# Optimization experiments

Measured on AMD Instinct MI355X. Metric: run time of the kernel, lower is better.

## Reference

```python
import jax, jax.numpy as jnp
import numpy as np

NPOINT = 1024
RADIUS = 0.2
NSAMPLE = 32
EPS = 1e-5


def farthest_point_sample(xyz, npoint):
    # xyz: [B, N, 3] -> [B, npoint] int32, deterministic start at index 0
    B, N, _ = xyz.shape

    def step(carry, _):
        dist, farthest = carry
        centroid = jnp.take_along_axis(xyz, farthest[:, None, None], axis=1)  # [B,1,3]
        d = jnp.sum((xyz - centroid) ** 2, axis=-1)  # [B,N]
        dist = jnp.minimum(dist, d)
        nxt = jnp.argmax(dist, axis=-1).astype(jnp.int32)
        return (dist, nxt), farthest

    init = (jnp.full((B, N), 1e10, dtype=xyz.dtype), jnp.zeros((B,), dtype=jnp.int32))
    _, idxs = jax.lax.scan(step, init, None, length=npoint)
    return idxs.T  # [B, npoint]


def query_ball_point(radius, nsample, xyz, new_xyz):
    # xyz: [B,N,3], new_xyz: [B,S,3] -> [B,S,nsample] int32
    N = xyz.shape[1]
    sqr = jnp.sum((new_xyz[:, :, None, :] - xyz[:, None, :, :]) ** 2, axis=-1)  # [B,S,N]
    ar = jnp.arange(N, dtype=jnp.int32)
    gidx = jnp.where(sqr > radius ** 2, N, ar[None, None, :])
    gidx = jnp.sort(gidx, axis=-1)[:, :, :nsample]  # sorts index values, matching torch
    first = gidx[:, :, :1]
    return jnp.where(gidx == N, first, gidx)


def mlp_layer(h, w, b, g, be, m, v):
    # h: [B, Cin, K, S]; 1x1 Conv2d + BatchNorm2d(eval) + ReLU
    h = jnp.einsum('oc,bcks->boks', w, h) + b[None, :, None, None]
    h = (h - m[None, :, None, None]) * (g[None, :, None, None] / jnp.sqrt(v[None, :, None, None] + EPS)) + be[None, :, None, None]
    return jax.nn.relu(h)


def setup_inputs() -> dict:
    key = jax.random.key(0)
    ks = jax.random.split(key, 24)
    inp = {
        'xyz': jax.random.normal(ks[0], (1, 16, 3, 4096), jnp.float32),
        'points': jax.random.normal(ks[1], (1, 16, 64, 4096), jnp.float32),
        'w0': jax.random.normal(ks[2], (64, 67), jnp.float32) * 0.1,
        'b0': jax.random.normal(ks[3], (64,), jnp.float32) * 0.1,
        'g0': jax.random.uniform(ks[4], (64,), jnp.float32),
        'be0': jax.random.normal(ks[5], (64,), jnp.float32) * 0.1,
        'm0': jax.random.normal(ks[6], (64,), jnp.float32) * 0.1,
        'v0': jax.random.uniform(ks[7], (64,), jnp.float32),
        'w1': jax.random.normal(ks[8], (64, 64), jnp.float32) * 0.1,
        'b1': jax.random.normal(ks[9], (64,), jnp.float32) * 0.1,
        'g1': jax.random.uniform(ks[10], (64,), jnp.float32),
        'be1': jax.random.normal(ks[11], (64,), jnp.float32) * 0.1,
        'm1': jax.random.normal(ks[12], (64,), jnp.float32) * 0.1,
        'v1': jax.random.uniform(ks[13], (64,), jnp.float32),
        'w2': jax.random.normal(ks[14], (128, 64), jnp.float32) * 0.1,
        'b2': jax.random.normal(ks[15], (128,), jnp.float32) * 0.1,
        'g2': jax.random.uniform(ks[16], (128,), jnp.float32),
        'be2': jax.random.normal(ks[17], (128,), jnp.float32) * 0.1,
        'm2': jax.random.normal(ks[18], (128,), jnp.float32) * 0.1,
        'v2': jax.random.uniform(ks[19], (128,), jnp.float32),
    }
    return inp


def reference(xyz, points, w0, b0, g0, be0, m0, v0, w1, b1, g1, be1, m1, v1, w2, b2, g2, be2, m2, v2):
    T, B, C, N = xyz.shape
    BT = T * B
    x = xyz.reshape(BT, C, N).transpose(0, 2, 1)          # [B', N, 3]
    p = points.reshape(BT, -1, N).transpose(0, 2, 1)      # [B', N, D]

    fps_idx = farthest_point_sample(x, NPOINT)            # [B', S]
    bidx = jnp.arange(BT)[:, None]
    new_xyz = x[bidx, fps_idx]                            # [B', S, 3]

    idx = query_ball_point(RADIUS, NSAMPLE, x, new_xyz)   # [B', S, K]
    b3 = jnp.arange(BT)[:, None, None]
    grouped_xyz = x[b3, idx]                              # [B', S, K, 3]
    grouped_norm = grouped_xyz - new_xyz[:, :, None, :]
    grouped_p = p[b3, idx]                                # [B', S, K, D]
    new_points = jnp.concatenate([grouped_norm, grouped_p], axis=-1)  # [B', S, K, 3+D]

    h = new_points.transpose(0, 3, 2, 1)                  # [B', 3+D, K, S]
    h = mlp_layer(h, w0, b0, g0, be0, m0, v0)
    h = mlp_layer(h, w1, b1, g1, be1, m1, v1)
    h = mlp_layer(h, w2, b2, g2, be2, m2, v2)
    out = jnp.max(h, axis=2)                              # [B', Cout, S]

    new_xyz_out = new_xyz.transpose(0, 2, 1).reshape(T, B, C, NPOINT)
    return new_xyz_out, out
```

## Files before the change

### kernel.cpp

```cpp
#include <hip/hip_runtime.h>
#include <hip/hip_bf16.h>

#define NPTS    4096
#define NBATCH  16
#define NPOINT  1024
#define NSAMPLE 32

typedef float v2f __attribute__((ext_vector_type(2)));

#define ROW_SHR1  0x111
#define ROW_SHR2  0x112
#define ROW_SHR4  0x114
#define ROW_SHR8  0x118
#define ROW_BC15  0x142
#define ROW_BC31  0x143

template<int CTRL>
__device__ __forceinline__ unsigned dpp_mov(unsigned v) {
    return (unsigned)__builtin_amdgcn_update_dpp(0, (int)v, CTRL, 0xF, 0xF, true);
}
template<int CTRL>
__device__ __forceinline__ float dpp_maxf(float v) {
    unsigned t = dpp_mov<CTRL>(__float_as_uint(v));
    return fmaxf(v, __uint_as_float(t));
}

__device__ void u_role(int g, const float* __restrict__ points,
                       const float* __restrict__ w0, float* __restrict__ U)
{
    const int b = g >> 12, p = g & (NPTS - 1);
    const float* pb = points + (size_t)b * 64 * NPTS + p;
    float in[64];
    #pragma unroll
    for (int c = 0; c < 64; ++c) in[c] = pb[c * NPTS];

    float* ug = U + (size_t)g * 64;
    for (int o4 = 0; o4 < 64; o4 += 4) {
        const float* r0 = w0 + (o4+0)*67 + 3;
        const float* r1 = w0 + (o4+1)*67 + 3;
        const float* r2 = w0 + (o4+2)*67 + 3;
        const float* r3 = w0 + (o4+3)*67 + 3;
        float a0 = 0.f, a1 = 0.f, a2 = 0.f, a3 = 0.f;
        #pragma unroll
        for (int c = 0; c < 64; ++c) {
            const float x = in[c];
            a0 = fmaf(r0[c], x, a0);
            a1 = fmaf(r1[c], x, a1);
            a2 = fmaf(r2[c], x, a2);
            a3 = fmaf(r3[c], x, a3);
        }
        *(float4*)(ug + o4) = make_float4(a0, a1, a2, a3);
    }
}

__device__ void setup_role(
    const float* __restrict__ w0, const float* __restrict__ b0,
    const float* __restrict__ g0, const float* __restrict__ be0,
    const float* __restrict__ m0, const float* __restrict__ v0,
    const float* __restrict__ w1, const float* __restrict__ b1,
    const float* __restrict__ g1, const float* __restrict__ be1,
    const float* __restrict__ m1, const float* __restrict__ v1,
    const float* __restrict__ b2, const float* __restrict__ g2,
    const float* __restrict__ be2, const float* __restrict__ m2,
    const float* __restrict__ v2, float* __restrict__ wp)
{
    const int t = threadIdx.x;
    for (int i = t; i < 3*64; i += 256) {
        int k = i >> 6, o = i & 63;
        wp[i] = w0[o*67 + k];
    }
    for (int i = t; i < 64*64; i += 256) {
        int o = i >> 6, k = i & 63;
        wp[192 + k*64 + o] = w1[i];
    }
    if (t < 64) {
        float s0 = g0[t] / sqrtf(v0[t] + 1e-5f);
        wp[4288 + t] = s0;
        wp[4352 + t] = (b0[t] - m0[t]) * s0 + be0[t];
        float s1 = g1[t] / sqrtf(v1[t] + 1e-5f);
        wp[4416 + t] = s1;
        wp[4480 + t] = (b1[t] - m1[t]) * s1 + be1[t];
    }
    if (t < 128) {
        float s2 = g2[t] / sqrtf(v2[t] + 1e-5f);
        wp[4544 + t] = s2;
        wp[4672 + t] = (b2[t] - m2[t]) * s2 + be2[t];
    }
}

__global__ __launch_bounds__(256) void fps_fused_kernel(
    const float* __restrict__ xyz, const float* __restrict__ points,
    const float* __restrict__ w0, const float* __restrict__ b0,
    const float* __restrict__ g0, const float* __restrict__ be0,
    const float* __restrict__ m0, const float* __restrict__ v0,
    const float* __restrict__ w1, const float* __restrict__ b1,
    const float* __restrict__ g1, const float* __restrict__ be1,
    const float* __restrict__ m1, const float* __restrict__ v1,
    const float* __restrict__ b2, const float* __restrict__ g2,
    const float* __restrict__ be2, const float* __restrict__ m2,
    const float* __restrict__ v2,
    float* __restrict__ newxyz, float* __restrict__ U, float* __restrict__ wp)
{
    #pragma clang fp contract(off)
    if (blockIdx.x >= 16) {
        if (blockIdx.x < 272) {
            u_role((blockIdx.x - 16) * 256 + threadIdx.x, points, w0, U);
        } else {
            setup_role(w0,b0,g0,be0,m0,v0, w1,b1,g1,be1,m1,v1,
                       b2,g2,be2,m2,v2, wp);
        }
        return;
    }

    const int b    = blockIdx.x;
    const int tid  = threadIdx.x;
    const int lane = tid & 63;
    const int w    = tid >> 6;
    const float* xb = xyz + (size_t)b * 3 * NPTS;

    __shared__ float4 P[NPTS];
    __shared__ unsigned long long slotk[2][4];
    __shared__ float4 slotc[2][4];

    v2f px2[8], py2[8], pz2[8], dist2[8];
    #pragma unroll
    for (int q = 0; q < 4; ++q) {
        const int n4 = tid * 16 + q * 4;
        float4 xs = *(const float4*)(xb + n4);
        float4 ys = *(const float4*)(xb + NPTS + n4);
        float4 zs = *(const float4*)(xb + 2*NPTS + n4);
        px2[2*q+0] = (v2f){xs.x, xs.y}; px2[2*q+1] = (v2f){xs.z, xs.w};
        py2[2*q+0] = (v2f){ys.x, ys.y}; py2[2*q+1] = (v2f){ys.z, ys.w};
        pz2[2*q+0] = (v2f){zs.x, zs.y}; pz2[2*q+1] = (v2f){zs.z, zs.w};
        P[n4+0] = make_float4(xs.x, ys.x, zs.x, 0.f);
        P[n4+1] = make_float4(xs.y, ys.y, zs.y, 0.f);
        P[n4+2] = make_float4(xs.z, ys.z, zs.z, 0.f);
        P[n4+3] = make_float4(xs.w, ys.w, zs.w, 0.f);
    }
    #pragma unroll
    for (int j = 0; j < 8; ++j) dist2[j] = (v2f){1e10f, 1e10f};
    __syncthreads();

    float4 c0 = P[0];
    float cx = c0.x, cy = c0.y, cz = c0.z;
    if (tid == 0) {
        newxyz[b*3*NPOINT + 0]        = cx;
        newxyz[b*3*NPOINT + NPOINT]   = cy;
        newxyz[b*3*NPOINT + 2*NPOINT] = cz;
    }

    for (int i = 1; i < NPOINT; ++i) {
        const int s = i & 1;
        const v2f cx2 = (v2f){cx, cx};
        const v2f cy2 = (v2f){cy, cy};
        const v2f cz2 = (v2f){cz, cz};
        float bv = -1.0f; int bj = 0;
        #pragma unroll
        for (int j2 = 0; j2 < 8; ++j2) {
            v2f dx = px2[j2] - cx2;
            v2f dy = py2[j2] - cy2;
            v2f dz = pz2[j2] - cz2;
            v2f xx = dx*dx, yy = dy*dy, zz = dz*dz;
            v2f dd = (xx + yy) + zz;
            v2f nd;
            nd.x = fminf(dist2[j2].x, dd.x);
            nd.y = fminf(dist2[j2].y, dd.y);
            dist2[j2] = nd;
            if (nd.x > bv) { bv = nd.x; bj = 2*j2; }
            if (nd.y > bv) { bv = nd.y; bj = 2*j2+1; }
        }
        const int myidx = (tid << 4) | bj;

        float wv = bv;
        wv = dpp_maxf<ROW_SHR1>(wv);
        wv = dpp_maxf<ROW_SHR2>(wv);
        wv = dpp_maxf<ROW_SHR4>(wv);
        wv = dpp_maxf<ROW_SHR8>(wv);
        wv = dpp_maxf<ROW_BC15>(wv);
        wv = dpp_maxf<ROW_BC31>(wv);
        float wmax = __uint_as_float(
            (unsigned)__builtin_amdgcn_readlane((int)__float_as_uint(wv), 63));
        unsigned long long mask = __ballot(bv == wmax);
        int L = (int)__builtin_ctzll(mask);
        int widx = __builtin_amdgcn_readlane(myidx, L);

        float4 cand = P[widx];
        if (lane == 0) {
            slotk[s][w] = ((unsigned long long)__float_as_uint(wmax) << 32) |
                          (unsigned long long)(unsigned)(~widx);
            slotc[s][w] = cand;
        }
        __syncthreads();

        unsigned long long k0 = slotk[s][0], k1 = slotk[s][1];
        unsigned long long k2 = slotk[s][2], k3 = slotk[s][3];
        float4 s0 = slotc[s][0], s1 = slotc[s][1];
        float4 s2 = slotc[s][2], s3 = slotc[s][3];
        bool b01 = k1 > k0;
        unsigned long long ka = b01 ? k1 : k0;
        float ax = b01 ? s1.x : s0.x, ay = b01 ? s1.y : s0.y, az = b01 ? s1.z : s0.z;
        bool b23 = k3 > k2;
        unsigned long long kb = b23 ? k3 : k2;
        float bx = b23 ? s3.x : s2.x, by = b23 ? s3.y : s2.y, bz = b23 ? s3.z : s2.z;
        bool ab = kb > ka;
        cx = ab ? bx : ax; cy = ab ? by : ay; cz = ab ? bz : az;

        if (tid == 0) {
            newxyz[b*3*NPOINT + i]            = cx;
            newxyz[b*3*NPOINT + NPOINT + i]   = cy;
            newxyz[b*3*NPOINT + 2*NPOINT + i] = cz;
        }
    }
}

__global__ __launch_bounds__(256) void ball_kernel(
    const float* __restrict__ xyz, const float* __restrict__ newxyz,
    int* __restrict__ ball_idx)
{
    const int gid  = blockIdx.x * 256 + threadIdx.x;
    const int wid  = gid >> 6;
    const int lane = threadIdx.x & 63;
    const int b    = wid >> 10;
    const int m    = wid & (NPOINT - 1);
    const float r2 = (float)(0.2 * 0.2);

    const float* xb = xyz + (size_t)b * 3 * NPTS;
    const float cx = newxyz[b*3*NPOINT + m];
    const float cy = newxyz[b*3*NPOINT + NPOINT + m];
    const float cz = newxyz[b*3*NPOINT + 2*NPOINT + m];
    int* out = ball_idx + (size_t)wid * NSAMPLE;

    int base = 0, first = 0;
    for (int c0 = 0; c0 < NPTS; c0 += 64) {
        const int n = c0 + lane;
        float dx = xb[n] - cx, dy = xb[NPTS+n] - cy, dz = xb[2*NPTS+n] - cz;
        float d = __fadd_rn(__fadd_rn(__fmul_rn(dx,dx), __fmul_rn(dy,dy)),
                            __fmul_rn(dz,dz));
        bool inb = (d <= r2);
        unsigned long long mask = __ballot(inb);
        if (base == 0 && mask != 0ull) first = c0 + (int)__builtin_ctzll(mask);
        int pos = base + __popcll(mask & ((1ull << lane) - 1ull));
        if (inb && pos < NSAMPLE) out[pos] = n;
        base += __popcll(mask);
        if (base >= NSAMPLE) break;
    }
    if (lane < NSAMPLE && lane >= base) out[lane] = first;
}

__global__ __launch_bounds__(256) void mlp_kernel(
    const float* __restrict__ xyz, const float* __restrict__ newxyz,
    const int* __restrict__ ball_idx, const float* __restrict__ U,
    const float* __restrict__ wp, const float* __restrict__ w2,
    float* __restrict__ out)
{
    const int col = blockIdx.x * 256 + threadIdx.x;
    const int m   = (col >> 5) & (NPOINT - 1);
    const int b   = col >> 15;
    const int p   = ball_idx[col];

    const float* xb = xyz + (size_t)b * 3 * NPTS;
    const float n0 = xb[p]          - newxyz[b*3*NPOINT + m];
    const float n1 = xb[NPTS + p]   - newxyz[b*3*NPOINT + NPOINT + m];
    const float n2 = xb[2*NPTS + p] - newxyz[b*3*NPOINT + 2*NPOINT + m];

    const float* w0t3 = wp;
    const float* w1t  = wp + 192;
    const float* sc0  = wp + 4288;
    const float* sh0  = wp + 4352;
    const float* sc1  = wp + 4416;
    const float* sh1  = wp + 4480;
    const float* sc2  = wp + 4544;
    const float* sh2  = wp + 4672;

    float h[64];
    const float4* Up = (const float4*)(U + ((size_t)((b << 12) | p)) * 64);
    #pragma unroll
    for (int q = 0; q < 16; ++q) {
        float4 u = Up[q];
        h[4*q+0] = u.x; h[4*q+1] = u.y; h[4*q+2] = u.z; h[4*q+3] = u.w;
    }
    #pragma unroll
    for (int o = 0; o < 64; ++o) h[o] = fmaf(w0t3[o],       n0, h[o]);
    #pragma unroll
    for (int o = 0; o < 64; ++o) h[o] = fmaf(w0t3[64 + o],  n1, h[o]);
    #pragma unroll
    for (int o = 0; o < 64; ++o) h[o] = fmaf(w0t3[128 + o], n2, h[o]);
    #pragma unroll
    for (int o = 0; o < 64; ++o)
        h[o] = fmaxf(fmaf(h[o], sc0[o], sh0[o]), 0.0f);

    float g[64];
    #pragma unroll
    for (int o = 0; o < 64; ++o) g[o] = 0.0f;
    #pragma unroll
    for (int k = 0; k < 64; ++k) {
        const float x = h[k];
        #pragma unroll
        for (int o = 0; o < 64; ++o) g[o] = fmaf(w1t[k*64 + o], x, g[o]);
    }
    #pragma unroll
    for (int o = 0; o < 64; ++o)
        g[o] = fmaxf(fmaf(g[o], sc1[o], sh1[o]), 0.0f);

    float* outb = out + (size_t)b * 128 * NPOINT + m;
    #pragma unroll 2
    for (int o = 0; o < 128; ++o) {
        float acc = 0.0f;
        const float* wr = w2 + o * 64;
        #pragma unroll
        for (int k = 0; k < 64; ++k) acc = fmaf(wr[k], g[k], acc);
        acc = fmaxf(fmaf(acc, sc2[o], sh2[o]), 0.0f);
        acc = dpp_maxf<ROW_SHR1>(acc);
        acc = dpp_maxf<ROW_SHR2>(acc);
        acc = dpp_maxf<ROW_SHR4>(acc);
        acc = dpp_maxf<ROW_SHR8>(acc);
        acc = dpp_maxf<ROW_BC15>(acc);
        if ((threadIdx.x & 31) == 31) outb[o * NPOINT] = acc;
    }
}

extern "C" void kernel_launch(void* const* d_in, const int* in_sizes, int n_in,
                              void* d_out, int out_size, void* d_ws, size_t ws_size,
                              hipStream_t stream)
{
    const float* xyz    = (const float*)d_in[0];
    const float* points = (const float*)d_in[1];
    const float* w0  = (const float*)d_in[2];
    const float* b0  = (const float*)d_in[3];
    const float* g0  = (const float*)d_in[4];
    const float* be0 = (const float*)d_in[5];
    const float* m0  = (const float*)d_in[6];
    const float* v0  = (const float*)d_in[7];
    const float* w1  = (const float*)d_in[8];
    const float* b1  = (const float*)d_in[9];
    const float* g1  = (const float*)d_in[10];
    const float* be1 = (const float*)d_in[11];
    const float* m1  = (const float*)d_in[12];
    const float* v1  = (const float*)d_in[13];
    const float* w2  = (const float*)d_in[14];
    const float* b2  = (const float*)d_in[15];
    const float* g2  = (const float*)d_in[16];
    const float* be2 = (const float*)d_in[17];
    const float* m2  = (const float*)d_in[18];
    const float* v2  = (const float*)d_in[19];

    float* out0 = (float*)d_out;
    float* out1 = out0 + NBATCH * 3 * NPOINT;

    float* U    = (float*)d_ws;
    int*   ball = (int*)((char*)d_ws + (size_t)NBATCH*NPTS*64*sizeof(float));
    float* wp   = (float*)((char*)ball + (size_t)NBATCH*NPOINT*NSAMPLE*sizeof(int));

    hipLaunchKernelGGL(fps_fused_kernel, dim3(273), dim3(256), 0, stream,
                       xyz, points, w0,b0,g0,be0,m0,v0, w1,b1,g1,be1,m1,v1,
                       b2,g2,be2,m2,v2, out0, U, wp);
    hipLaunchKernelGGL(ball_kernel, dim3(NBATCH*NPOINT/4), dim3(256), 0, stream,
                       xyz, out0, ball);
    hipLaunchKernelGGL(mlp_kernel,  dim3(NBATCH*NPOINT*NSAMPLE/256), dim3(256), 0, stream,
                       xyz, out0, ball, U, wp, w2, out1);
}
```

Baseline: 1.003 ms.

## Fuse FPS, ball query and MLP into one persistent producer-consumer kernel

Merges the three kernels into a single persistent launch. Sixteen blocks run farthest-point sampling at raised priority and publish progress counters. The other 240 blocks compute U and the weight setup, wait at a grid barrier, then take work items from an atomic queue. Each item spin-waits until its centroids are ready, then does the ball query into shared memory and the MLP. This overlaps the serial FPS phase with the ball query and MLP, and removes the ball-index round trip through global memory. In exchange it depends on all 256 blocks being co-resident and on cross-block atomics and spin-waits.

Result: slower. 1.047 ms (+4.3%).

```diff
diff --git a/kernel.cpp b/kernel.cpp
--- a/kernel.cpp
+++ b/kernel.cpp
@@ -7,6 +7,7 @@
 #define NSAMPLE 32
 
 typedef float v2f __attribute__((ext_vector_type(2)));
+typedef unsigned long long ull;
 
 #define ROW_SHR1  0x111
 #define ROW_SHR2  0x112
@@ -24,6 +25,11 @@
     unsigned t = dpp_mov<CTRL>(__float_as_uint(v));
     return fmaxf(v, __uint_as_float(t));
 }
+
+#define CTRL_DONE  16
+#define CTRL_QHEAD 17
+#define NCONS      240
+#define NITEMS     2048
 
 __device__ void u_role(int g, const float* __restrict__ points,
                        const float* __restrict__ w0, float* __restrict__ U)
@@ -88,234 +94,270 @@
     }
 }
 
-__global__ __launch_bounds__(256) void fps_fused_kernel(
+__global__ __launch_bounds__(256) void fused_kernel(
     const float* __restrict__ xyz, const float* __restrict__ points,
     const float* __restrict__ w0, const float* __restrict__ b0,
     const float* __restrict__ g0, const float* __restrict__ be0,
-    const float* __restrict__ m0, const float* __restrict__ v0,
+    const float* __restrict__ m0w, const float* __restrict__ v0,
     const float* __restrict__ w1, const float* __restrict__ b1,
     const float* __restrict__ g1, const float* __restrict__ be1,
-    const float* __restrict__ m1, const float* __restrict__ v1,
-    const float* __restrict__ b2, const float* __restrict__ g2,
-    const float* __restrict__ be2, const float* __restrict__ m2,
-    const float* __restrict__ v2,
-    float* __restrict__ newxyz, float* __restrict__ U, float* __restrict__ wp)
+    const float* __restrict__ m1w, const float* __restrict__ v1,
+    const float* __restrict__ w2, const float* __restrict__ b2,
+    const float* __restrict__ g2, const float* __restrict__ be2,
+    const float* __restrict__ m2w, const float* __restrict__ v2,
+    float* __restrict__ newxyz, float* __restrict__ out1,
+    float* __restrict__ U, float* __restrict__ wp, int* __restrict__ ctrl)
 {
     #pragma clang fp contract(off)
-    if (blockIdx.x >= 16) {
-        if (blockIdx.x < 272) {
-            u_role((blockIdx.x - 16) * 256 + threadIdx.x, points, w0, U);
-        } else {
-            setup_role(w0,b0,g0,be0,m0,v0, w1,b1,g1,be1,m1,v1,
-                       b2,g2,be2,m2,v2, wp);
+    __shared__ __align__(16) char smem[65728];
+    __shared__ int item_s;
+
+    if (blockIdx.x < 16) {
+        __builtin_amdgcn_s_setprio(2);
+        float4* P     = reinterpret_cast<float4*>(smem);
+        ull*    slotk = reinterpret_cast<ull*>(smem + 65536);
+        float4* slotc = reinterpret_cast<float4*>(smem + 65600);
+
+        const int b    = blockIdx.x;
+        const int tid  = threadIdx.x;
+        const int lane = tid & 63;
+        const int w    = tid >> 6;
+        const float* xb = xyz + (size_t)b * 3 * NPTS;
+
+        v2f px2[8], py2[8], pz2[8], dist2[8];
+        #pragma unroll
+        for (int q = 0; q < 4; ++q) {
+            const int n4 = tid * 16 + q * 4;
+            float4 xs = *(const float4*)(xb + n4);
+            float4 ys = *(const float4*)(xb + NPTS + n4);
+            float4 zs = *(const float4*)(xb + 2*NPTS + n4);
+            px2[2*q+0] = (v2f){xs.x, xs.y}; px2[2*q+1] = (v2f){xs.z, xs.w};
+            py2[2*q+0] = (v2f){ys.x, ys.y}; py2[2*q+1] = (v2f){ys.z, ys.w};
+            pz2[2*q+0] = (v2f){zs.x, zs.y}; pz2[2*q+1] = (v2f){zs.z, zs.w};
+            P[n4+0] = make_float4(xs.x, ys.x, zs.x, 0.f);
+            P[n4+1] = make_float4(xs.y, ys.y, zs.y, 0.f);
+            P[n4+2] = make_float4(xs.z, ys.z, zs.z, 0.f);
+            P[n4+3] = make_float4(xs.w, ys.w, zs.w, 0.f);
+        }
+        #pragma unroll
+        for (int j = 0; j < 8; ++j) dist2[j] = (v2f){1e10f, 1e10f};
+        __syncthreads();
+
+        float4 c0 = P[0];
+        float cx = c0.x, cy = c0.y, cz = c0.z;
+        if (tid == 0) {
+            newxyz[b*3*NPOINT + 0]        = cx;
+            newxyz[b*3*NPOINT + NPOINT]   = cy;
+            newxyz[b*3*NPOINT + 2*NPOINT] = cz;
+        }
+
+        for (int i = 1; i < NPOINT; ++i) {
+            const int s = i & 1;
+            const v2f cx2 = (v2f){cx, cx};
+            const v2f cy2 = (v2f){cy, cy};
+            const v2f cz2 = (v2f){cz, cz};
+            float bv = -1.0f; int bj = 0;
+            #pragma unroll
+            for (int j2 = 0; j2 < 8; ++j2) {
+                v2f dx = px2[j2] - cx2;
+                v2f dy = py2[j2] - cy2;
+                v2f dz = pz2[j2] - cz2;
+                v2f xx = dx*dx, yy = dy*dy, zz = dz*dz;
+                v2f dd = (xx + yy) + zz;
+                v2f nd;
+                nd.x = fminf(dist2[j2].x, dd.x);
+                nd.y = fminf(dist2[j2].y, dd.y);
+                dist2[j2] = nd;
+                if (nd.x > bv) { bv = nd.x; bj = 2*j2; }
+                if (nd.y > bv) { bv = nd.y; bj = 2*j2+1; }
+            }
+            const int myidx = (tid << 4) | bj;
+
+            float wv = bv;
+            wv = dpp_maxf<ROW_SHR1>(wv);
+            wv = dpp_maxf<ROW_SHR2>(wv);
+            wv = dpp_maxf<ROW_SHR4>(wv);
+            wv = dpp_maxf<ROW_SHR8>(wv);
+            wv = dpp_maxf<ROW_BC15>(wv);
+            wv = dpp_maxf<ROW_BC31>(wv);
+            float wmax = __uint_as_float(
+                (unsigned)__builtin_amdgcn_readlane((int)__float_as_uint(wv), 63));
+            ull mask = __ballot(bv == wmax);
+            int L = (int)__builtin_ctzll(mask);
+            int widx = __builtin_amdgcn_readlane(myidx, L);
+
+            float4 cand = P[widx];
+            if (lane == 0) {
+                slotk[s*4 + w] = ((ull)__float_as_uint(wmax) << 32) |
+                                 (ull)(unsigned)(~widx);
+                slotc[s*4 + w] = cand;
+            }
+            __syncthreads();
+
+            ull k0 = slotk[s*4+0], k1 = slotk[s*4+1];
+            ull k2 = slotk[s*4+2], k3 = slotk[s*4+3];
+            float4 s0 = slotc[s*4+0], s1 = slotc[s*4+1];
+            float4 s2 = slotc[s*4+2], s3 = slotc[s*4+3];
+            bool b01 = k1 > k0;
+            ull ka = b01 ? k1 : k0;
+            float ax = b01 ? s1.x : s0.x, ay = b01 ? s1.y : s0.y, az = b01 ? s1.z : s0.z;
+            bool b23 = k3 > k2;
+            ull kb = b23 ? k3 : k2;
+            float bx = b23 ? s3.x : s2.x, by = b23 ? s3.y : s2.y, bz = b23 ? s3.z : s2.z;
+            bool ab = kb > ka;
+            cx = ab ? bx : ax; cy = ab ? by : ay; cz = ab ? bz : az;
+
+            if (tid == 0) {
+                newxyz[b*3*NPOINT + i]            = cx;
+                newxyz[b*3*NPOINT + NPOINT + i]   = cy;
+                newxyz[b*3*NPOINT + 2*NPOINT + i] = cz;
+                if ((i & 15) == 15)
+                    __hip_atomic_store(&ctrl[b], i, __ATOMIC_RELEASE,
+                                       __HIP_MEMORY_SCOPE_AGENT);
+            }
         }
         return;
     }
 
-    const int b    = blockIdx.x;
-    const int tid  = threadIdx.x;
-    const int lane = tid & 63;
-    const int w    = tid >> 6;
-    const float* xb = xyz + (size_t)b * 3 * NPTS;
-
-    __shared__ float4 P[NPTS];
-    __shared__ unsigned long long slotk[2][4];
-    __shared__ float4 slotc[2][4];
-
-    v2f px2[8], py2[8], pz2[8], dist2[8];
-    #pragma unroll
-    for (int q = 0; q < 4; ++q) {
-        const int n4 = tid * 16 + q * 4;
-        float4 xs = *(const float4*)(xb + n4);
-        float4 ys = *(const float4*)(xb + NPTS + n4);
-        float4 zs = *(const float4*)(xb + 2*NPTS + n4);
-        px2[2*q+0] = (v2f){xs.x, xs.y}; px2[2*q+1] = (v2f){xs.z, xs.w};
-        py2[2*q+0] = (v2f){ys.x, ys.y}; py2[2*q+1] = (v2f){ys.z, ys.w};
-        pz2[2*q+0] = (v2f){zs.x, zs.y}; pz2[2*q+1] = (v2f){zs.z, zs.w};
-        P[n4+0] = make_float4(xs.x, ys.x, zs.x, 0.f);
-        P[n4+1] = make_float4(xs.y, ys.y, zs.y, 0.f);
-        P[n4+2] = make_float4(xs.z, ys.z, zs.z, 0.f);
-        P[n4+3] = make_float4(xs.w, ys.w, zs.w, 0.f);
-    }
-    #pragma unroll
-    for (int j = 0; j < 8; ++j) dist2[j] = (v2f){1e10f, 1e10f};
+    __builtin_amdgcn_s_setprio(0);
+    const int cb  = blockIdx.x - 16;
+    const int tid = threadIdx.x;
+
+    for (int g = cb * 256 + tid; g < NBATCH * NPTS; g += NCONS * 256)
+        u_role(g, points, w0, U);
+    if (cb == 0)
+        setup_role(w0,b0,g0,be0,m0w,v0, w1,b1,g1,be1,m1w,v1,
+                   b2,g2,be2,m2w,v2, wp);
     __syncthreads();
-
-    float4 c0 = P[0];
-    float cx = c0.x, cy = c0.y, cz = c0.z;
     if (tid == 0) {
-        newxyz[b*3*NPOINT + 0]        = cx;
-        newxyz[b*3*NPOINT + NPOINT]   = cy;
-        newxyz[b*3*NPOINT + 2*NPOINT] = cz;
-    }
-
-    for (int i = 1; i < NPOINT; ++i) {
-        const int s = i & 1;
-        const v2f cx2 = (v2f){cx, cx};
-        const v2f cy2 = (v2f){cy, cy};
-        const v2f cz2 = (v2f){cz, cz};
-        float bv = -1.0f; int bj = 0;
-        #pragma unroll
-        for (int j2 = 0; j2 < 8; ++j2) {
-            v2f dx = px2[j2] - cx2;
-            v2f dy = py2[j2] - cy2;
-            v2f dz = pz2[j2] - cz2;
-            v2f xx = dx*dx, yy = dy*dy, zz = dz*dz;
-            v2f dd = (xx + yy) + zz;
-            v2f nd;
-            nd.x = fminf(dist2[j2].x, dd.x);
-            nd.y = fminf(dist2[j2].y, dd.y);
-            dist2[j2] = nd;
-            if (nd.x > bv) { bv = nd.x; bj = 2*j2; }
-            if (nd.y > bv) { bv = nd.y; bj = 2*j2+1; }
-        }
-        const int myidx = (tid << 4) | bj;
-
-        float wv = bv;
-        wv = dpp_maxf<ROW_SHR1>(wv);
-        wv = dpp_maxf<ROW_SHR2>(wv);
-        wv = dpp_maxf<ROW_SHR4>(wv);
-        wv = dpp_maxf<ROW_SHR8>(wv);
-        wv = dpp_maxf<ROW_BC15>(wv);
-        wv = dpp_maxf<ROW_BC31>(wv);
-        float wmax = __uint_as_float(
-            (unsigned)__builtin_amdgcn_readlane((int)__float_as_uint(wv), 63));
-        unsigned long long mask = __ballot(bv == wmax);
-        int L = (int)__builtin_ctzll(mask);
-        int widx = __builtin_amdgcn_readlane(myidx, L);
-
-        float4 cand = P[widx];
-        if (lane == 0) {
-            slotk[s][w] = ((unsigned long long)__float_as_uint(wmax) << 32) |
-                          (unsigned long long)(unsigned)(~widx);
-            slotc[s][w] = cand;
-        }
+        __hip_atomic_fetch_add(&ctrl[CTRL_DONE], 1, __ATOMIC_ACQ_REL,
+                               __HIP_MEMORY_SCOPE_AGENT);
+        while (__hip_atomic_load(&ctrl[CTRL_DONE], __ATOMIC_ACQUIRE,
+                                 __HIP_MEMORY_SCOPE_AGENT) < NCONS)
+            __builtin_amdgcn_s_sleep(8);
+    }
+    __syncthreads();
+    asm volatile("s_dcache_inv" ::: "memory");
+
+    float* wpl   = reinterpret_cast<float*>(smem);
+    int*   ballL = reinterpret_cast<int*>(smem + 19200);
+    float* cxl   = reinterpret_cast<float*>(smem + 20224);
+
+    for (int i2 = tid; i2 < 4800; i2 += 256) wpl[i2] = wp[i2];
+    __syncthreads();
+
+    const float r2   = (float)(0.2 * 0.2);
+    const int   lane = tid & 63;
+    const int   wv   = tid >> 6;
+
+    for (;;) {
+        if (tid == 0)
+            item_s = __hip_atomic_fetch_add(&ctrl[CTRL_QHEAD], 1,
+                                            __ATOMIC_RELAXED,
+                                            __HIP_MEMORY_SCOPE_AGENT);
         __syncthreads();
-
-        unsigned long long k0 = slotk[s][0], k1 = slotk[s][1];
-        unsigned long long k2 = slotk[s][2], k3 = slotk[s][3];
-        float4 s0 = slotc[s][0], s1 = slotc[s][1];
-        float4 s2 = slotc[s][2], s3 = slotc[s][3];
-        bool b01 = k1 > k0;
-        unsigned long long ka = b01 ? k1 : k0;
-        float ax = b01 ? s1.x : s0.x, ay = b01 ? s1.y : s0.y, az = b01 ? s1.z : s0.z;
-        bool b23 = k3 > k2;
-        unsigned long long kb = b23 ? k3 : k2;
-        float bx = b23 ? s3.x : s2.x, by = b23 ? s3.y : s2.y, bz = b23 ? s3.z : s2.z;
-        bool ab = kb > ka;
-        cx = ab ? bx : ax; cy = ab ? by : ay; cz = ab ? bz : az;
+        const int w = item_s;
+        if (w >= NITEMS) break;
+        const int b  = w & 15;
+        const int m0 = (w >> 4) << 3;
 
         if (tid == 0) {
-            newxyz[b*3*NPOINT + i]            = cx;
-            newxyz[b*3*NPOINT + NPOINT + i]   = cy;
-            newxyz[b*3*NPOINT + 2*NPOINT + i] = cz;
-        }
-    }
-}
-
-__global__ __launch_bounds__(256) void ball_kernel(
-    const float* __restrict__ xyz, const float* __restrict__ newxyz,
-    int* __restrict__ ball_idx)
-{
-    const int gid  = blockIdx.x * 256 + threadIdx.x;
-    const int wid  = gid >> 6;
-    const int lane = threadIdx.x & 63;
-    const int b    = wid >> 10;
-    const int m    = wid & (NPOINT - 1);
-    const float r2 = (float)(0.2 * 0.2);
-
-    const float* xb = xyz + (size_t)b * 3 * NPTS;
-    const float cx = newxyz[b*3*NPOINT + m];
-    const float cy = newxyz[b*3*NPOINT + NPOINT + m];
-    const float cz = newxyz[b*3*NPOINT + 2*NPOINT + m];
-    int* out = ball_idx + (size_t)wid * NSAMPLE;
-
-    int base = 0, first = 0;
-    for (int c0 = 0; c0 < NPTS; c0 += 64) {
-        const int n = c0 + lane;
-        float dx = xb[n] - cx, dy = xb[NPTS+n] - cy, dz = xb[2*NPTS+n] - cz;
-        float d = __fadd_rn(__fadd_rn(__fmul_rn(dx,dx), __fmul_rn(dy,dy)),
-                            __fmul_rn(dz,dz));
-        bool inb = (d <= r2);
-        unsigned long long mask = __ballot(inb);
-        if (base == 0 && mask != 0ull) first = c0 + (int)__builtin_ctzll(mask);
-        int pos = base + __popcll(mask & ((1ull << lane) - 1ull));
-        if (inb && pos < NSAMPLE) out[pos] = n;
-        base += __popcll(mask);
-        if (base >= NSAMPLE) break;
-    }
-    if (lane < NSAMPLE && lane >= base) out[lane] = first;
-}
-
-__global__ __launch_bounds__(256) void mlp_kernel(
-    const float* __restrict__ xyz, const float* __restrict__ newxyz,
-    const int* __restrict__ ball_idx, const float* __restrict__ U,
-    const float* __restrict__ wp, const float* __restrict__ w2,
-    float* __restrict__ out)
-{
-    const int col = blockIdx.x * 256 + threadIdx.x;
-    const int m   = (col >> 5) & (NPOINT - 1);
-    const int b   = col >> 15;
-    const int p   = ball_idx[col];
-
-    const float* xb = xyz + (size_t)b * 3 * NPTS;
-    const float n0 = xb[p]          - newxyz[b*3*NPOINT + m];
-    const float n1 = xb[NPTS + p]   - newxyz[b*3*NPOINT + NPOINT + m];
-    const float n2 = xb[2*NPTS + p] - newxyz[b*3*NPOINT + 2*NPOINT + m];
-
-    const float* w0t3 = wp;
-    const float* w1t  = wp + 192;
-    const float* sc0  = wp + 4288;
-    const float* sh0  = wp + 4352;
-    const float* sc1  = wp + 4416;
-    const float* sh1  = wp + 4480;
-    const float* sc2  = wp + 4544;
-    const float* sh2  = wp + 4672;
-
-    float h[64];
-    const float4* Up = (const float4*)(U + ((size_t)((b << 12) | p)) * 64);
-    #pragma unroll
-    for (int q = 0; q < 16; ++q) {
-        float4 u = Up[q];
-        h[4*q+0] = u.x; h[4*q+1] = u.y; h[4*q+2] = u.z; h[4*q+3] = u.w;
-    }
-    #pragma unroll
-    for (int o = 0; o < 64; ++o) h[o] = fmaf(w0t3[o],       n0, h[o]);
-    #pragma unroll
-    for (int o = 0; o < 64; ++o) h[o] = fmaf(w0t3[64 + o],  n1, h[o]);
-    #pragma unroll
-    for (int o = 0; o < 64; ++o) h[o] = fmaf(w0t3[128 + o], n2, h[o]);
-    #pragma unroll
-    for (int o = 0; o < 64; ++o)
-        h[o] = fmaxf(fmaf(h[o], sc0[o], sh0[o]), 0.0f);
-
-    float g[64];
-    #pragma unroll
-    for (int o = 0; o < 64; ++o) g[o] = 0.0f;
-    #pragma unroll
-    for (int k = 0; k < 64; ++k) {
-        const float x = h[k];
-        #pragma unroll
-        for (int o = 0; o < 64; ++o) g[o] = fmaf(w1t[k*64 + o], x, g[o]);
-    }
-    #pragma unroll
-    for (int o = 0; o < 64; ++o)
-        g[o] = fmaxf(fmaf(g[o], sc1[o], sh1[o]), 0.0f);
-
-    float* outb = out + (size_t)b * 128 * NPOINT + m;
-    #pragma unroll 2
-    for (int o = 0; o < 128; ++o) {
-        float acc = 0.0f;
-        const float* wr = w2 + o * 64;
-        #pragma unroll
-        for (int k = 0; k < 64; ++k) acc = fmaf(wr[k], g[k], acc);
-        acc = fmaxf(fmaf(acc, sc2[o], sh2[o]), 0.0f);
-        acc = dpp_maxf<ROW_SHR1>(acc);
-        acc = dpp_maxf<ROW_SHR2>(acc);
-        acc = dpp_maxf<ROW_SHR4>(acc);
-        acc = dpp_maxf<ROW_SHR8>(acc);
-        acc = dpp_maxf<ROW_BC15>(acc);
-        if ((threadIdx.x & 31) == 31) outb[o * NPOINT] = acc;
+            while (__hip_atomic_load(&ctrl[b], __ATOMIC_ACQUIRE,
+                                     __HIP_MEMORY_SCOPE_AGENT) < m0 + 7)
+                __builtin_amdgcn_s_sleep(16);
+        }
+        __syncthreads();
+
+        if (tid < 24) {
+            int c = tid >> 3, j = tid & 7;
+            cxl[tid] = newxyz[b*3*NPOINT + c*NPOINT + m0 + j];
+        }
+        __syncthreads();
+
+        const float* xb = xyz + (size_t)b * 3 * NPTS;
+        for (int cc = 0; cc < 2; ++cc) {
+            const int lm = wv*2 + cc;
+            const float ccx = cxl[lm], ccy = cxl[8+lm], ccz = cxl[16+lm];
+            int* outi = ballL + lm * NSAMPLE;
+            int base = 0, first = 0;
+            for (int c0 = 0; c0 < NPTS; c0 += 64) {
+                const int n = c0 + lane;
+                float dx = xb[n] - ccx, dy = xb[NPTS+n] - ccy, dz = xb[2*NPTS+n] - ccz;
+                float d = __fadd_rn(__fadd_rn(__fmul_rn(dx,dx), __fmul_rn(dy,dy)),
+                                    __fmul_rn(dz,dz));
+                bool inb = (d <= r2);
+                ull mask = __ballot(inb);
+                if (base == 0 && mask != 0ull) first = c0 + (int)__builtin_ctzll(mask);
+                int pos = base + __popcll(mask & ((1ull << lane) - 1ull));
+                if (inb && pos < NSAMPLE) outi[pos] = n;
+                base += __popcll(mask);
+                if (base >= NSAMPLE) break;
+            }
+            if (lane < NSAMPLE && lane >= base) outi[lane] = first;
+        }
+        __syncthreads();
+
+        const int lm5 = tid >> 5;
+        const int m   = m0 + lm5;
+        const int p   = ballL[tid];
+        const float n0 = xb[p]          - cxl[lm5];
+        const float n1 = xb[NPTS + p]   - cxl[8 + lm5];
+        const float n2 = xb[2*NPTS + p] - cxl[16 + lm5];
+
+        const float* w0t3 = wpl;
+        const float* w1t  = wpl + 192;
+        const float* sc0  = wpl + 4288;
+        const float* sh0  = wpl + 4352;
+        const float* sc1  = wpl + 4416;
+        const float* sh1  = wpl + 4480;
+        const float* sc2  = wpl + 4544;
+        const float* sh2  = wpl + 4672;
+
+        float h[64];
+        const float4* Up = (const float4*)(U + ((size_t)((b << 12) | p)) * 64);
+        #pragma unroll
+        for (int q = 0; q < 16; ++q) {
+            float4 u = Up[q];
+            h[4*q+0] = u.x; h[4*q+1] = u.y; h[4*q+2] = u.z; h[4*q+3] = u.w;
+        }
+        #pragma unroll
+        for (int o = 0; o < 64; ++o) h[o] = fmaf(w0t3[o],       n0, h[o]);
+        #pragma unroll
+        for (int o = 0; o < 64; ++o) h[o] = fmaf(w0t3[64 + o],  n1, h[o]);
+        #pragma unroll
+        for (int o = 0; o < 64; ++o) h[o] = fmaf(w0t3[128 + o], n2, h[o]);
+        #pragma unroll
+        for (int o = 0; o < 64; ++o)
+            h[o] = fmaxf(fmaf(h[o], sc0[o], sh0[o]), 0.0f);
+
+        float gg[64];
+        #pragma unroll
+        for (int o = 0; o < 64; ++o) gg[o] = 0.0f;
+        #pragma unroll
+        for (int k = 0; k < 64; ++k) {
+            const float x = h[k];
+            #pragma unroll
+            for (int o = 0; o < 64; ++o) gg[o] = fmaf(w1t[k*64 + o], x, gg[o]);
+        }
+        #pragma unroll
+        for (int o = 0; o < 64; ++o)
+            gg[o] = fmaxf(fmaf(gg[o], sc1[o], sh1[o]), 0.0f);
+
+        float* outb = out1 + (size_t)b * 128 * NPOINT + m;
+        #pragma unroll 2
+        for (int o = 0; o < 128; ++o) {
+            float acc = 0.0f;
+            const float* wr = w2 + o * 64;
+            #pragma unroll
+            for (int k = 0; k < 64; ++k) acc = fmaf(wr[k], gg[k], acc);
+            acc = fmaxf(fmaf(acc, sc2[o], sh2[o]), 0.0f);
+            acc = dpp_maxf<ROW_SHR1>(acc);
+            acc = dpp_maxf<ROW_SHR2>(acc);
+            acc = dpp_maxf<ROW_SHR4>(acc);
+            acc = dpp_maxf<ROW_SHR8>(acc);
+            acc = dpp_maxf<ROW_BC15>(acc);
+            if ((tid & 31) == 31) outb[o * NPOINT] = acc;
+        }
     }
 }
 
@@ -347,15 +389,12 @@
     float* out0 = (float*)d_out;
     float* out1 = out0 + NBATCH * 3 * NPOINT;
 
-    float* U    = (float*)d_ws;
-    int*   ball = (int*)((char*)d_ws + (size_t)NBATCH*NPTS*64*sizeof(float));
-    float* wp   = (float*)((char*)ball + (size_t)NBATCH*NPOINT*NSAMPLE*sizeof(int));
-
-    hipLaunchKernelGGL(fps_fused_kernel, dim3(273), dim3(256), 0, stream,
+    int*   ctrl = (int*)d_ws;
+    float* U    = (float*)((char*)d_ws + 256);
+    float* wp   = (float*)((char*)d_ws + 256 + (size_t)NBATCH*NPTS*64*sizeof(float));
+
+    hipMemsetAsync(d_ws, 0, 256, stream);
+    hipLaunchKernelGGL(fused_kernel, dim3(256), dim3(256), 0, stream,
                        xyz, points, w0,b0,g0,be0,m0,v0, w1,b1,g1,be1,m1,v1,
-                       b2,g2,be2,m2,v2, out0, U, wp);
-    hipLaunchKernelGGL(ball_kernel, dim3(NBATCH*NPOINT/4), dim3(256), 0, stream,
-                       xyz, out0, ball);
-    hipLaunchKernelGGL(mlp_kernel,  dim3(NBATCH*NPOINT*NSAMPLE/256), dim3(256), 0, stream,
-                       xyz, out0, ball, U, wp, w2, out1);
-}
+                       w2,b2,g2,be2,m2,v2, out0, out1, U, wp, ctrl);
+}
```
